# Kernel tuning notes

Hardware: AMD Instinct MI355X
Metric: run time of the kernel (lower is better)

## Reference

```python
import jax, jax.numpy as jnp
import numpy as np

N = 100000   # nodes
E = 1600000  # edges
F = 128      # num_features
H = 128      # hidden width
G = 64       # graphs in batch (target_size)
C = 10       # output_channels


def setup_inputs() -> dict:
    key = jax.random.key(0)
    ks = jax.random.split(key, 16)
    s = 0.05
    inp = {
        "x": jax.random.normal(ks[0], (N, F), jnp.float32),
        "edge_index": jax.random.randint(ks[1], (2, E), 0, N, jnp.int32),
        "batch": jnp.sort(jax.random.randint(ks[2], (N,), 0, G, jnp.int32)),
        "target_size": G,
        # GraphConv layer params: lin_rel (weight+bias) applied to aggregated
        # neighbors, lin_root (weight, no bias) applied to self features.
        "W1_rel": jax.random.normal(ks[3], (H, F), jnp.float32) * s,
        "b1_rel": jnp.zeros((H,), jnp.float32),
        "W1_root": jax.random.normal(ks[4], (H, F), jnp.float32) * s,
        "W2_rel": jax.random.normal(ks[5], (H, H), jnp.float32) * s,
        "b2_rel": jnp.zeros((H,), jnp.float32),
        "W2_root": jax.random.normal(ks[6], (H, H), jnp.float32) * s,
        "W3_rel": jax.random.normal(ks[7], (H, H), jnp.float32) * s,
        "b3_rel": jnp.zeros((H,), jnp.float32),
        "W3_root": jax.random.normal(ks[8], (H, H), jnp.float32) * s,
        "Wl1": jax.random.normal(ks[9], (64, H), jnp.float32) * s,
        "bl1": jnp.zeros((64,), jnp.float32),
        "Wl2": jax.random.normal(ks[10], (C, 64), jnp.float32) * s,
        "bl2": jnp.zeros((C,), jnp.float32),
    }
    return inp


def _graph_conv(x, src, dst, W_rel, b_rel, W_root):
    # PyG GraphConv (aggr='add'): out_i = W_rel @ sum_{j->i} x_j + b_rel + W_root @ x_i
    agg = jax.ops.segment_sum(x[src], dst, num_segments=N)  # [N, F_in]
    return agg @ W_rel.T + b_rel + x @ W_root.T


def reference(x, edge_index, batch, target_size,
              W1_rel, b1_rel, W1_root,
              W2_rel, b2_rel, W2_root,
              W3_rel, b3_rel, W3_root,
              Wl1, bl1, Wl2, bl2):
    src, dst = edge_index[0], edge_index[1]
    h = jax.nn.relu(_graph_conv(x, src, dst, W1_rel, b1_rel, W1_root))
    h = jax.nn.relu(_graph_conv(h, src, dst, W2_rel, b2_rel, W2_root))
    h = jax.nn.relu(_graph_conv(h, src, dst, W3_rel, b3_rel, W3_root))
    # global_mean_pool over graph ids
    sums = jax.ops.segment_sum(h, batch, num_segments=target_size)        # [G, H]
    cnts = jax.ops.segment_sum(jnp.ones((N, 1), h.dtype), batch,
                               num_segments=target_size)                  # [G, 1]
    pooled = sums / jnp.maximum(cnts, 1.0)
    h = jax.nn.relu(pooled @ Wl1.T + bl1)
    return jax.nn.log_softmax(h @ Wl2.T + bl2, axis=-1)
```

## Files before the change

### kernel.cpp

```cpp
#include <hip/hip_runtime.h>

#define N_NODES 100000
#define NPAD    100096
#define N_EDGES 1600000
#define FDIM 128
#define GDIM 64
#define CDIM 10

#define BSH   9
#define BSIZE 512
#define NB    196
#define EPB   8192
#define EPB_C 6250

typedef unsigned short us16;
typedef us16 usx4 __attribute__((ext_vector_type(4)));
typedef us16 usx8 __attribute__((ext_vector_type(8)));
typedef short bfrag __attribute__((ext_vector_type(8)));
typedef float f32x4 __attribute__((ext_vector_type(4)));

__device__ __forceinline__ float bf2f(us16 u) {
  return __uint_as_float(((unsigned)u) << 16);
}
__device__ __forceinline__ us16 f2bf(float f) {
  unsigned u = __float_as_uint(f);
  u += 0x7FFFu + ((u >> 16) & 1u);
  return (us16)(u >> 16);
}

#define XB 6250
__global__ __launch_bounds__(256) void k_prep(
    const float* __restrict__ x, us16* __restrict__ xb,
    const float* __restrict__ Wrel1, const float* __restrict__ Wroot1,
    const float* __restrict__ Wrel2, const float* __restrict__ Wroot2,
    const float* __restrict__ Wrel3, const float* __restrict__ Wroot3,
    us16* __restrict__ Wp, float* __restrict__ pooled,
    const int* __restrict__ edst, int* __restrict__ bcnt) {
  int bx = blockIdx.x, tid = threadIdx.x;
  if (bx < XB) {
    size_t i = ((size_t)bx * 256 + tid) * 8;
    float4 a = *(const float4*)(x + i);
    float4 b = *(const float4*)(x + i + 4);
    usx8 o;
    o[0]=f2bf(a.x); o[1]=f2bf(a.y); o[2]=f2bf(a.z); o[3]=f2bf(a.w);
    o[4]=f2bf(b.x); o[5]=f2bf(b.y); o[6]=f2bf(b.z); o[7]=f2bf(b.w);
    *(usx8*)(xb + i) = o;
  } else if (bx < XB + 384) {
    int wb = bx - XB;
    int l = wb >> 7;
    const float* Wrel  = (l == 0) ? Wrel1  : (l == 1) ? Wrel2  : Wrel3;
    const float* Wroot = (l == 0) ? Wroot1 : (l == 1) ? Wroot2 : Wroot3;
    int idx = (wb & 127) * 256 + tid;
    int k = idx >> 7;
    int c = idx & 127;
    float v = (k < 128) ? Wrel[c * 128 + k] : Wroot[c * 128 + k - 128];
    Wp[(size_t)l * 32768 + (((k >> 3) * 128 + c) << 3) + (k & 7)] = f2bf(v);
  } else if (bx == XB + 384) {
    for (int i = tid; i < GDIM * FDIM; i += 256) pooled[i] = 0.f;
  } else {
    __shared__ int h[NB];
    int cb = bx - (XB + 385);
    for (int i = tid; i < NB; i += 256) h[i] = 0;
    __syncthreads();
    int s0 = cb * EPB;
    int e0 = s0 + EPB; if (e0 > N_EDGES) e0 = N_EDGES;
    for (int i = s0 + tid; i < e0; i += 256) atomicAdd(&h[edst[i] >> BSH], 1);
    __syncthreads();
    for (int i = tid; i < NB; i += 256)
      if (h[i]) atomicAdd(&bcnt[i], h[i]);
  }
}

__device__ __forceinline__ void scan_bcnt(const int* __restrict__ bcnt,
                                          int* sm , int* boffL ,
                                          int tid) {
  int v = (tid < NB) ? bcnt[tid] : 0;
  if (tid < 256) sm[tid] = v;
  __syncthreads();
  for (int off = 1; off < 256; off <<= 1) {
    int t = (tid >= off && tid < 256) ? sm[tid - off] : 0;
    __syncthreads();
    if (tid < 256) sm[tid] += t;
    __syncthreads();
  }
  if (tid < NB) boffL[tid] = sm[tid] - v;
  __syncthreads();
}

__global__ __launch_bounds__(1024) void k_bscatter(
    const int* __restrict__ src, const int* __restrict__ dst,
    const int* __restrict__ bcnt, int* __restrict__ bcursor,
    int* __restrict__ ebuf) {
  __shared__ int sm[256];
  __shared__ int boffL[NB];
  __shared__ int h[NB];
  __shared__ int base[NB];
  __shared__ int lc[NB];
  int tid = threadIdx.x;
  for (int i = tid; i < NB; i += 1024) h[i] = 0;
  scan_bcnt(bcnt, sm, boffL, tid);
  int s0 = blockIdx.x * EPB_C;
  int e0 = s0 + EPB_C; if (e0 > N_EDGES) e0 = N_EDGES;
  for (int i = s0 + tid; i < e0; i += 1024) atomicAdd(&h[dst[i] >> BSH], 1);
  __syncthreads();
  for (int i = tid; i < NB; i += 1024) {
    base[i] = h[i] ? (boffL[i] + atomicAdd(&bcursor[i], h[i])) : 0;
    lc[i] = 0;
  }
  __syncthreads();
  for (int i = s0 + tid; i < e0; i += 1024) {
    int d = dst[i];
    int b = d >> BSH;
    int lp = atomicAdd(&lc[b], 1);
    ebuf[base[b] + lp] = (src[i] << BSH) | (d & (BSIZE - 1));
  }
}

__global__ __launch_bounds__(1024) void k_bucket_csr(
    const int* __restrict__ ebuf, const int* __restrict__ bcnt,
    int* __restrict__ row_ptr, int* __restrict__ csr_src) {
  __shared__ int sm[256];
  __shared__ int boffL[NB];
  __shared__ int hist[BSIZE];
  __shared__ int cur[BSIZE];
  __shared__ int se[2];
  int b = blockIdx.x, tid = threadIdx.x;
  if (tid < BSIZE) hist[tid] = 0;
  scan_bcnt(bcnt, sm, boffL, tid);
  if (tid == 0) {
    se[0] = boffL[b];
    se[1] = (b + 1 < NB) ? boffL[b + 1] : N_EDGES;
    if (b == 0) row_ptr[N_NODES] = N_EDGES;
  }
  __syncthreads();
  int eoff = se[0], ecnt = se[1] - se[0];
  int base = b * BSIZE;
  for (int i = tid; i < ecnt; i += 1024)
    atomicAdd(&hist[ebuf[eoff + i] & (BSIZE - 1)], 1);
  __syncthreads();
  for (int d = 1; d < BSIZE; d <<= 1) {
    int idx = (tid + 1) * (d << 1) - 1;
    if (idx < BSIZE) hist[idx] += hist[idx - d];
    __syncthreads();
  }
  if (tid == 0) hist[BSIZE - 1] = 0;
  __syncthreads();
  for (int d = BSIZE >> 1; d >= 1; d >>= 1) {
    int idx = (tid + 1) * (d << 1) - 1;
    if (idx < BSIZE) {
      int t = hist[idx - d];
      hist[idx - d] = hist[idx];
      hist[idx] += t;
    }
    __syncthreads();
  }
  if (tid < BSIZE) {
    int node = base + tid;
    if (node < N_NODES) row_ptr[node] = eoff + hist[tid];
    cur[tid] = hist[tid];
  }
  __syncthreads();
  for (int i = tid; i < ecnt; i += 1024) {
    int e = ebuf[eoff + i];
    int lp = atomicAdd(&cur[e & (BSIZE - 1)], 1);
    csr_src[eoff + lp] = e >> BSH;
  }
}

#define ASTR 136
#define LROWS 128
__global__ __launch_bounds__(512) void k_layer(
    const us16* __restrict__ hin, const us16* __restrict__ Wp,
    const float* __restrict__ bias, const int* __restrict__ row_ptr,
    const int* __restrict__ csr_src, us16* __restrict__ out,
    const int* __restrict__ batch, float* __restrict__ pooled) {
  __shared__ us16 As[LROWS * ASTR];
  int tid = threadIdx.x;
  int node0 = blockIdx.x * LROWS;
  int slot = tid >> 4;
  int lane16 = tid & 15;
  const us16* gbase = hin + lane16 * 8;

#pragma unroll 1
  for (int rnd = 0; rnd < 4; ++rnd) {
    int node = node0 + rnd * 32 + slot;
    float a0 = 0.f, a1 = 0.f, a2 = 0.f, a3 = 0.f;
    float a4 = 0.f, a5 = 0.f, a6 = 0.f, a7 = 0.f;
    if (node < N_NODES) {
      int s = row_ptr[node], e = row_ptr[node + 1];
      int p = s;
      for (; p + 4 <= e; p += 4) {
        int j0 = csr_src[p], j1 = csr_src[p + 1];
        int j2 = csr_src[p + 2], j3 = csr_src[p + 3];
        usx8 v0 = *(const usx8*)(gbase + (size_t)j0 * FDIM);
        usx8 v1 = *(const usx8*)(gbase + (size_t)j1 * FDIM);
        usx8 v2 = *(const usx8*)(gbase + (size_t)j2 * FDIM);
        usx8 v3 = *(const usx8*)(gbase + (size_t)j3 * FDIM);
        a0 += bf2f(v0[0]) + bf2f(v1[0]) + bf2f(v2[0]) + bf2f(v3[0]);
        a1 += bf2f(v0[1]) + bf2f(v1[1]) + bf2f(v2[1]) + bf2f(v3[1]);
        a2 += bf2f(v0[2]) + bf2f(v1[2]) + bf2f(v2[2]) + bf2f(v3[2]);
        a3 += bf2f(v0[3]) + bf2f(v1[3]) + bf2f(v2[3]) + bf2f(v3[3]);
        a4 += bf2f(v0[4]) + bf2f(v1[4]) + bf2f(v2[4]) + bf2f(v3[4]);
        a5 += bf2f(v0[5]) + bf2f(v1[5]) + bf2f(v2[5]) + bf2f(v3[5]);
        a6 += bf2f(v0[6]) + bf2f(v1[6]) + bf2f(v2[6]) + bf2f(v3[6]);
        a7 += bf2f(v0[7]) + bf2f(v1[7]) + bf2f(v2[7]) + bf2f(v3[7]);
      }
      for (; p < e; ++p) {
        int j = csr_src[p];
        usx8 v = *(const usx8*)(gbase + (size_t)j * FDIM);
        a0 += bf2f(v[0]); a1 += bf2f(v[1]); a2 += bf2f(v[2]); a3 += bf2f(v[3]);
        a4 += bf2f(v[4]); a5 += bf2f(v[5]); a6 += bf2f(v[6]); a7 += bf2f(v[7]);
      }
    }
    usx8 o;
    o[0] = f2bf(a0); o[1] = f2bf(a1); o[2] = f2bf(a2); o[3] = f2bf(a3);
    o[4] = f2bf(a4); o[5] = f2bf(a5); o[6] = f2bf(a6); o[7] = f2bf(a7);
    *(usx8*)&As[(rnd * 32 + slot) * ASTR + lane16 * 8] = o;
  }
  __syncthreads();

  int wave = tid >> 6, lane = tid & 63;
  int m = lane & 15, quad = lane >> 4;
  size_t rowA = (size_t)(node0 + wave * 16 + m);
  const us16* baseH = hin + rowA * FDIM + quad * 8;
  const us16* aldsb = &As[(wave * 16 + m) * ASTR + quad * 8];
  f32x4 acc[8];
#pragma unroll
  for (int t = 0; t < 8; ++t) acc[t] = (f32x4){0.f, 0.f, 0.f, 0.f};

#pragma unroll 1
  for (int c = 0; c < 8; ++c) {
    bfrag a;
    if (c < 4) a = *(const bfrag*)(aldsb + c * 32);
    else       a = *(const bfrag*)(baseH + (c - 4) * 32);
    int kq = c * 4 + quad;
    const us16* wbase = Wp + (((size_t)kq * 128 + m) << 3);
#pragma unroll
    for (int t = 0; t < 8; ++t) {
      bfrag b = *(const bfrag*)(wbase + t * 128);
      acc[t] = __builtin_amdgcn_mfma_f32_16x16x32_bf16(a, b, acc[t], 0, 0, 0);
    }
  }
  int w16 = node0 + wave * 16;
  int orow0 = w16 + quad * 4;
  if (pooled == nullptr) {
#pragma unroll
    for (int t = 0; t < 8; ++t) {
      int col = t * 16 + m;
      float bv = bias[col];
#pragma unroll
      for (int i = 0; i < 4; ++i) {
        int r = orow0 + i;
        if (r < N_NODES)
          out[(size_t)r * FDIM + col] = f2bf(fmaxf(acc[t][i] + bv, 0.f));
      }
    }
  } else {
    int rlast = w16 + 15;
    int gfirst = batch[(w16 < N_NODES) ? w16 : (N_NODES - 1)];
    int glast  = batch[(rlast < N_NODES) ? rlast : (N_NODES - 1)];
    bool uniform = (gfirst == glast) && (rlast < N_NODES);
    if (uniform) {
#pragma unroll
      for (int t = 0; t < 8; ++t) {
        int col = t * 16 + m;
        float bv = bias[col];
        float v = fmaxf(acc[t][0] + bv, 0.f) + fmaxf(acc[t][1] + bv, 0.f) +
                  fmaxf(acc[t][2] + bv, 0.f) + fmaxf(acc[t][3] + bv, 0.f);
        v += __shfl_xor(v, 16);
        v += __shfl_xor(v, 32);
        if (quad == 0) atomicAdd(&pooled[gfirst * FDIM + col], v);
      }
    } else {
      int g[4];
#pragma unroll
      for (int i = 0; i < 4; ++i) {
        int r = orow0 + i;
        g[i] = batch[(r < N_NODES) ? r : (N_NODES - 1)];
      }
#pragma unroll
      for (int t = 0; t < 8; ++t) {
        int col = t * 16 + m;
        float bv = bias[col];
#pragma unroll
        for (int i = 0; i < 4; ++i) {
          int r = orow0 + i;
          if (r < N_NODES)
            atomicAdd(&pooled[g[i] * FDIM + col], fmaxf(acc[t][i] + bv, 0.f));
        }
      }
    }
  }
}

__global__ __launch_bounds__(128) void k_head(
    const float* __restrict__ pooled, const int* __restrict__ batch,
    const float* __restrict__ Wl1, const float* __restrict__ bl1,
    const float* __restrict__ Wl2, const float* __restrict__ bl2,
    float* __restrict__ out) {
  int g = blockIdx.x;
  __shared__ int sb[2];
  __shared__ float p[128];
  __shared__ float h1[64];
  __shared__ float logit[CDIM];
  if (threadIdx.x < 2) {
    int key = g + (int)threadIdx.x;
    int lo = 0, hi = N_NODES;
    while (lo < hi) {
      int mid = (lo + hi) >> 1;
      if (batch[mid] < key) lo = mid + 1; else hi = mid;
    }
    sb[threadIdx.x] = lo;
  }
  __syncthreads();
  float cnt = (float)(sb[1] - sb[0]);
  p[threadIdx.x] = pooled[g * FDIM + threadIdx.x] / fmaxf(cnt, 1.f);
  __syncthreads();
  if (threadIdx.x < 64) {
    float acc = bl1[threadIdx.x];
    for (int k = 0; k < 128; ++k) acc += p[k] * Wl1[threadIdx.x * 128 + k];
    h1[threadIdx.x] = fmaxf(acc, 0.f);
  }
  __syncthreads();
  if (threadIdx.x < CDIM) {
    float acc = bl2[threadIdx.x];
    for (int k = 0; k < 64; ++k) acc += h1[k] * Wl2[threadIdx.x * 64 + k];
    logit[threadIdx.x] = acc;
  }
  __syncthreads();
  if (threadIdx.x == 0) {
    float m = -1e30f;
    for (int c = 0; c < CDIM; ++c) m = fmaxf(m, logit[c]);
    float s = 0.f;
    for (int c = 0; c < CDIM; ++c) s += expf(logit[c] - m);
    float ls = logf(s);
    for (int c = 0; c < CDIM; ++c) out[g * CDIM + c] = logit[c] - m - ls;
  }
}

extern "C" void kernel_launch(void* const* d_in, const int* in_sizes, int n_in,
                              void* d_out, int out_size, void* d_ws, size_t ws_size,
                              hipStream_t stream) {
  const float* x      = (const float*)d_in[0];
  const int* edge_idx = (const int*)d_in[1];
  const int* batch    = (const int*)d_in[2];
  const float* W1_rel  = (const float*)d_in[4];
  const float* b1_rel  = (const float*)d_in[5];
  const float* W1_root = (const float*)d_in[6];
  const float* W2_rel  = (const float*)d_in[7];
  const float* b2_rel  = (const float*)d_in[8];
  const float* W2_root = (const float*)d_in[9];
  const float* W3_rel  = (const float*)d_in[10];
  const float* b3_rel  = (const float*)d_in[11];
  const float* W3_root = (const float*)d_in[12];
  const float* Wl1     = (const float*)d_in[13];
  const float* bl1     = (const float*)d_in[14];
  const float* Wl2     = (const float*)d_in[15];
  const float* bl2     = (const float*)d_in[16];
  const int* esrc = edge_idx;
  const int* edst = edge_idx + N_EDGES;

  char* ws = (char*)d_ws;
  size_t off = 0;
  auto alloc = [&](size_t bytes) {
    void* p = ws + off;
    off += (bytes + 255) & ~(size_t)255;
    return p;
  };
  int* row_ptr  = (int*)alloc((N_NODES + 1) * sizeof(int));
  int* bc2      = (int*)alloc(2 * NB * sizeof(int));
  int* csr_src  = (int*)alloc(N_EDGES * sizeof(int));
  us16* xb      = (us16*)alloc((size_t)NPAD * FDIM * sizeof(us16));
  us16* hA      = (us16*)alloc((size_t)NPAD * FDIM * sizeof(us16));
  us16* hB      = (us16*)alloc((size_t)NPAD * FDIM * sizeof(us16));
  us16* Wp      = (us16*)alloc(3 * 32768 * sizeof(us16));
  float* pooled = (float*)alloc(GDIM * FDIM * sizeof(float));
  int* bcnt    = bc2;
  int* bcursor = bc2 + NB;
  int* ebuf     = (int*)hA;

  hipMemsetAsync(bc2, 0, 2 * NB * sizeof(int), stream);

  k_prep<<<XB + 384 + 1 + NB, 256, 0, stream>>>(
      x, xb, W1_rel, W1_root, W2_rel, W2_root, W3_rel, W3_root, Wp, pooled,
      edst, bcnt);

  k_bscatter<<<(N_EDGES + EPB_C - 1) / EPB_C, 1024, 0, stream>>>(
      esrc, edst, bcnt, bcursor, ebuf);
  k_bucket_csr<<<NB, 1024, 0, stream>>>(ebuf, bcnt, row_ptr, csr_src);

  int lgrid = NPAD / LROWS;
  k_layer<<<lgrid, 512, 0, stream>>>(xb, Wp,         b1_rel, row_ptr, csr_src,
                                     hA, batch, nullptr);
  k_layer<<<lgrid, 512, 0, stream>>>(hA, Wp + 32768, b2_rel, row_ptr, csr_src,
                                     hB, batch, nullptr);
  k_layer<<<lgrid, 512, 0, stream>>>(hB, Wp + 65536, b3_rel, row_ptr, csr_src,
                                     hA, batch, pooled);

  k_head<<<GDIM, 128, 0, stream>>>(pooled, batch, Wl1, bl1, Wl2, bl2, (float*)d_out);
}
```

Measured before the change: 428.2 us.

## Build CSR via global degree atomics and direct scatter instead of bucket sort

Replaces the two-pass bucketed counting sort for the CSR with per-node degree counting by global atomics in the prep kernel, a per-bucket scan kernel that writes row pointers, and a single scatter kernel that places each edge using an atomic cursor per destination. This removes the intermediate edge buffer pass and one kernel's worth of work. In exchange it adds contended global atomics and uncoalesced random writes, and the neighbor order within each row becomes nondeterministic.

```diff
diff --git a/kernel.cpp b/kernel.cpp
--- a/kernel.cpp
+++ b/kernel.cpp
@@ -11,7 +11,6 @@
 #define BSIZE 512
 #define NB    196
 #define EPB   8192
-#define EPB_C 6250
 
 typedef unsigned short us16;
 typedef us16 usx4 __attribute__((ext_vector_type(4)));
@@ -35,7 +34,8 @@
     const float* __restrict__ Wrel2, const float* __restrict__ Wroot2,
     const float* __restrict__ Wrel3, const float* __restrict__ Wroot3,
     us16* __restrict__ Wp, float* __restrict__ pooled,
-    const int* __restrict__ edst, int* __restrict__ bcnt) {
+    const int* __restrict__ edst, int* __restrict__ bcnt,
+    int* __restrict__ deg) {
   int bx = blockIdx.x, tid = threadIdx.x;
   if (bx < XB) {
     size_t i = ((size_t)bx * 256 + tid) * 8;
@@ -64,7 +64,11 @@
     __syncthreads();
     int s0 = cb * EPB;
     int e0 = s0 + EPB; if (e0 > N_EDGES) e0 = N_EDGES;
-    for (int i = s0 + tid; i < e0; i += 256) atomicAdd(&h[edst[i] >> BSH], 1);
+    for (int i = s0 + tid; i < e0; i += 256) {
+      int d = edst[i];
+      atomicAdd(&h[d >> BSH], 1);
+      atomicAdd(&deg[d], 1);
+    }
     __syncthreads();
     for (int i = tid; i < NB; i += 256)
       if (h[i]) atomicAdd(&bcnt[i], h[i]);
@@ -87,83 +91,49 @@
   __syncthreads();
 }
 
-__global__ __launch_bounds__(1024) void k_bscatter(
-    const int* __restrict__ src, const int* __restrict__ dst,
-    const int* __restrict__ bcnt, int* __restrict__ bcursor,
-    int* __restrict__ ebuf) {
+__global__ __launch_bounds__(512) void k_rowptr(
+    const int* __restrict__ bcnt, const int* __restrict__ deg,
+    int* __restrict__ row_ptr, int* __restrict__ cur) {
   __shared__ int sm[256];
   __shared__ int boffL[NB];
-  __shared__ int h[NB];
-  __shared__ int base[NB];
-  __shared__ int lc[NB];
-  int tid = threadIdx.x;
-  for (int i = tid; i < NB; i += 1024) h[i] = 0;
+  __shared__ int sc[BSIZE];
+  int b = blockIdx.x, tid = threadIdx.x;
   scan_bcnt(bcnt, sm, boffL, tid);
-  int s0 = blockIdx.x * EPB_C;
-  int e0 = s0 + EPB_C; if (e0 > N_EDGES) e0 = N_EDGES;
-  for (int i = s0 + tid; i < e0; i += 1024) atomicAdd(&h[dst[i] >> BSH], 1);
-  __syncthreads();
-  for (int i = tid; i < NB; i += 1024) {
-    base[i] = h[i] ? (boffL[i] + atomicAdd(&bcursor[i], h[i])) : 0;
-    lc[i] = 0;
-  }
-  __syncthreads();
-  for (int i = s0 + tid; i < e0; i += 1024) {
-    int d = dst[i];
-    int b = d >> BSH;
-    int lp = atomicAdd(&lc[b], 1);
-    ebuf[base[b] + lp] = (src[i] << BSH) | (d & (BSIZE - 1));
-  }
-}
-
-__global__ __launch_bounds__(1024) void k_bucket_csr(
-    const int* __restrict__ ebuf, const int* __restrict__ bcnt,
-    int* __restrict__ row_ptr, int* __restrict__ csr_src) {
-  __shared__ int sm[256];
-  __shared__ int boffL[NB];
-  __shared__ int hist[BSIZE];
-  __shared__ int cur[BSIZE];
-  __shared__ int se[2];
-  int b = blockIdx.x, tid = threadIdx.x;
-  if (tid < BSIZE) hist[tid] = 0;
-  scan_bcnt(bcnt, sm, boffL, tid);
-  if (tid == 0) {
-    se[0] = boffL[b];
-    se[1] = (b + 1 < NB) ? boffL[b + 1] : N_EDGES;
-    if (b == 0) row_ptr[N_NODES] = N_EDGES;
-  }
-  __syncthreads();
-  int eoff = se[0], ecnt = se[1] - se[0];
-  int base = b * BSIZE;
-  for (int i = tid; i < ecnt; i += 1024)
-    atomicAdd(&hist[ebuf[eoff + i] & (BSIZE - 1)], 1);
-  __syncthreads();
-  for (int d = 1; d < BSIZE; d <<= 1) {
-    int idx = (tid + 1) * (d << 1) - 1;
-    if (idx < BSIZE) hist[idx] += hist[idx - d];
-    __syncthreads();
-  }
-  if (tid == 0) hist[BSIZE - 1] = 0;
-  __syncthreads();
-  for (int d = BSIZE >> 1; d >= 1; d >>= 1) {
-    int idx = (tid + 1) * (d << 1) - 1;
+  int node = b * BSIZE + tid;
+  int d = (node < N_NODES) ? deg[node] : 0;
+  sc[tid] = d;
+  __syncthreads();
+  for (int dd = 1; dd < BSIZE; dd <<= 1) {
+    int idx = (tid + 1) * (dd << 1) - 1;
+    if (idx < BSIZE) sc[idx] += sc[idx - dd];
+    __syncthreads();
+  }
+  if (tid == 0) sc[BSIZE - 1] = 0;
+  __syncthreads();
+  for (int dd = BSIZE >> 1; dd >= 1; dd >>= 1) {
+    int idx = (tid + 1) * (dd << 1) - 1;
     if (idx < BSIZE) {
-      int t = hist[idx - d];
-      hist[idx - d] = hist[idx];
-      hist[idx] += t;
-    }
-    __syncthreads();
-  }
-  if (tid < BSIZE) {
-    int node = base + tid;
-    if (node < N_NODES) row_ptr[node] = eoff + hist[tid];
-    cur[tid] = hist[tid];
-  }
-  __syncthreads();
-  for (int i = tid; i < ecnt; i += 1024) {
-    int e = ebuf[eoff + i];
-    int lp = atomicAdd(&cur[e & (BSIZE - 1)], 1);
-    csr_src[eoff + lp] = e >> BSH;
+      int t = sc[idx - dd];
+      sc[idx - dd] = sc[idx];
+      sc[idx] += t;
+    }
+    __syncthreads();
+  }
+  if (node < N_NODES) {
+    int rp = boffL[b] + sc[tid];
+    row_ptr[node] = rp;
+    cur[node] = rp;
+  }
+  if (b == 0 && tid == 0) row_ptr[N_NODES] = N_EDGES;
+}
+
+__global__ __launch_bounds__(1024) void k_scatter(
+    const int* __restrict__ src, const int* __restrict__ dst,
+    int* __restrict__ cur, int* __restrict__ csr_src) {
+  int i = blockIdx.x * 1024 + threadIdx.x;
+  if (i < N_EDGES) {
+    int pos = atomicAdd(&cur[dst[i]], 1);
+    csr_src[pos] = src[i];
   }
 }
 
@@ -368,26 +338,25 @@
     return p;
   };
   int* row_ptr  = (int*)alloc((N_NODES + 1) * sizeof(int));
-  int* bc2      = (int*)alloc(2 * NB * sizeof(int));
   int* csr_src  = (int*)alloc(N_EDGES * sizeof(int));
   us16* xb      = (us16*)alloc((size_t)NPAD * FDIM * sizeof(us16));
   us16* hA      = (us16*)alloc((size_t)NPAD * FDIM * sizeof(us16));
   us16* hB      = (us16*)alloc((size_t)NPAD * FDIM * sizeof(us16));
   us16* Wp      = (us16*)alloc(3 * 32768 * sizeof(us16));
   float* pooled = (float*)alloc(GDIM * FDIM * sizeof(float));
-  int* bcnt    = bc2;
-  int* bcursor = bc2 + NB;
-  int* ebuf     = (int*)hA;
-
-  hipMemsetAsync(bc2, 0, 2 * NB * sizeof(int), stream);
+  int* bcnt = (int*)hA;
+  int* deg  = bcnt + NB;
+  int* cur  = deg + N_NODES;
+
+  hipMemsetAsync(bcnt, 0, (NB + N_NODES) * sizeof(int), stream);
 
   k_prep<<<XB + 384 + 1 + NB, 256, 0, stream>>>(
       x, xb, W1_rel, W1_root, W2_rel, W2_root, W3_rel, W3_root, Wp, pooled,
-      edst, bcnt);
-
-  k_bscatter<<<(N_EDGES + EPB_C - 1) / EPB_C, 1024, 0, stream>>>(
-      esrc, edst, bcnt, bcursor, ebuf);
-  k_bucket_csr<<<NB, 1024, 0, stream>>>(ebuf, bcnt, row_ptr, csr_src);
+      edst, bcnt, deg);
+
+  k_rowptr<<<NB, 512, 0, stream>>>(bcnt, deg, row_ptr, cur);
+  k_scatter<<<(N_EDGES + 1023) / 1024, 1024, 0, stream>>>(
+      esrc, edst, cur, csr_src);
 
   int lgrid = NPAD / LROWS;
   k_layer<<<lgrid, 512, 0, stream>>>(xb, Wp,         b1_rel, row_ptr, csr_src,
```

Result: slower. 589.7 us (+37.7%).
